# Kernel tuning notes

Measured on AMD Instinct MI355X. Metric: run time of the kernel, lower is better.

## Reference

```python
import jax, jax.numpy as jnp
import numpy as np

B, T, S, H = 4, 2048, 2048, 1024


def setup_inputs() -> dict:
    key = jax.random.key(0)
    k1, k2, k3, k4, k5, k6 = jax.random.split(key, 6)
    scale_w = 1.0 / np.sqrt(H)  # roughly nn.Linear init scale
    return {
        "tar": jax.random.normal(k1, (B, T, H), jnp.float32),
        "src": jax.random.normal(k2, (B, S, H), jnp.float32),
        "ori_src": jax.random.normal(k3, (B, S, H), jnp.float32),
        "Wq": jax.random.normal(k4, (H, H), jnp.float32) * scale_w,
        "Wk": jax.random.normal(k5, (H, H), jnp.float32) * scale_w,
        "Wv": jax.random.normal(k6, (H, H), jnp.float32) * scale_w,
    }


def reference(tar, src, ori_src, Wq, Wk, Wv):
    # nn.Linear(bias=False): y = x @ W.T
    q = src @ Wq.T        # (B, S, H)
    k = tar @ Wk.T        # (B, T, H)
    v = ori_src @ Wv.T    # (B, S, H)
    scaling = jnp.asarray(H ** 0.5, q.dtype)
    # scores[b,t,s] = q[b,s] . k[b,t] / sqrt(H); torch softmax was over dim=-2 (the S axis)
    scores = jnp.einsum('bsh,bth->bts', q, k) / scaling  # (B, T, S)
    attn = jax.nn.softmax(scores, axis=-1)               # softmax over src positions s
    context = jnp.einsum('bts,bsh->bth', attn, v)        # (B, T, H)
    return context, attn
```

## Files before the change

### kernel.cpp

```cpp
#include <hip/hip_runtime.h>

#define BB 4
#define TT 2048
#define SS 2048
#define HH 1024

typedef unsigned short u16;
typedef __attribute__((ext_vector_type(4))) unsigned short u16x4;
typedef __attribute__((ext_vector_type(8))) short bf16x8;
typedef __attribute__((ext_vector_type(4))) float f32x4;

__device__ __forceinline__ u16 f2bf(float f) {
    union { float f; unsigned u; } a; a.f = f;
    unsigned r = a.u + 0x7fffu + ((a.u >> 16) & 1u);
    return (u16)(r >> 16);
}

__device__ __forceinline__ void stage_bf16(const u16* gbase, int ld, int row0, int k0,
                                           u16* lds, int tid) {
#pragma unroll
    for (int c = 0; c < 2; ++c) {
        int g = c * 256 + tid;
        int row = g >> 2, col = g & 3;
        const u16* gp = gbase + (size_t)(row0 + row) * ld + k0 + col * 8;
        u16* lp = lds + (size_t)(c * 256 + (tid & ~63)) * 8;
        __builtin_amdgcn_global_load_lds((__attribute__((address_space(1))) const void*)gp,
                                         (__attribute__((address_space(3))) void*)lp,
                                         16, 0, 0);
    }
}

__device__ __forceinline__ void stage_f32(const float* gbase, int ld, int row0, int k0,
                                          u16* lds, int tid) {
#pragma unroll
    for (int c = 0; c < 4; ++c) {
        int f = c * 256 + tid;
        int row = f >> 3, c4 = f & 7;
        const float4 v = *(const float4*)(gbase + (size_t)(row0 + row) * ld + k0 + c4 * 4);
        u16x4 o;
        o.x = f2bf(v.x); o.y = f2bf(v.y); o.z = f2bf(v.z); o.w = f2bf(v.w);
        *(u16x4*)(lds + row * 32 + c4 * 4) = o;
    }
}

__device__ __forceinline__ void mfma_step(const u16* As, const u16* Bs,
                                          f32x4 acc[4][4], int tid) {
    int lane = tid & 63, quad = lane >> 4, l16 = lane & 15;
    int wm = (tid >> 6) & 1, wn = tid >> 7;
    const u16* Ab = As + (wm * 64 + l16) * 32 + quad * 8;
    const u16* Bb = Bs + (wn * 64 + l16) * 32 + quad * 8;
    bf16x8 af[4], bfr[4];
#pragma unroll
    for (int i = 0; i < 4; ++i) af[i] = *(const bf16x8*)(Ab + i * 512);
#pragma unroll
    for (int j = 0; j < 4; ++j) bfr[j] = *(const bf16x8*)(Bb + j * 512);
#pragma unroll
    for (int i = 0; i < 4; ++i)
#pragma unroll
        for (int j = 0; j < 4; ++j)
            acc[i][j] = __builtin_amdgcn_mfma_f32_16x16x32_bf16(af[i], bfr[j], acc[i][j], 0, 0, 0);
}

__device__ __forceinline__ void zero_acc(f32x4 acc[4][4]) {
#pragma unroll
    for (int i = 0; i < 4; ++i)
#pragma unroll
        for (int j = 0; j < 4; ++j)
            acc[i][j] = (f32x4){0.f, 0.f, 0.f, 0.f};
}

__global__ __launch_bounds__(256) void cvt_kernel(const float* __restrict__ in,
                                                  u16* __restrict__ out) {
    int i = (blockIdx.x * 256 + threadIdx.x) * 4;
    float4 v = *(const float4*)(in + i);
    u16x4 o;
    o.x = f2bf(v.x); o.y = f2bf(v.y); o.z = f2bf(v.z); o.w = f2bf(v.w);
    *(u16x4*)(out + i) = o;
}

template <int AF32>
__global__ __launch_bounds__(256) void proj_kernel(const float* __restrict__ F0,
                                                   const float* __restrict__ F1,
                                                   const float* __restrict__ F2,
                                                   const u16* __restrict__ A0,
                                                   const u16* __restrict__ A1,
                                                   const u16* __restrict__ A2,
                                                   const u16* __restrict__ W0,
                                                   const u16* __restrict__ W1,
                                                   const u16* __restrict__ W2,
                                                   u16* __restrict__ qb,
                                                   u16* __restrict__ kb,
                                                   u16* __restrict__ vT,
                                                   int zbase) {
    __shared__ u16 As[128 * 32];
    __shared__ u16 Bs[128 * 32];
    const int z = zbase + blockIdx.z;
    const float* AF = (z == 0) ? F0 : (z == 1) ? F1 : F2;
    const u16* AB = (z == 0) ? A0 : (z == 1) ? A1 : A2;
    const u16* W = (z == 0) ? W0 : (z == 1) ? W1 : W2;
    const int bm = blockIdx.y * 128, bn = blockIdx.x * 128;
    const int tid = threadIdx.x;

    f32x4 acc[4][4];
    zero_acc(acc);
    for (int k0 = 0; k0 < HH; k0 += 32) {
        if (AF32) stage_f32(AF, HH, bm, k0, As, tid);
        else      stage_bf16(AB, HH, bm, k0, As, tid);
        stage_bf16(W, HH, bn, k0, Bs, tid);
        __syncthreads();
        mfma_step(As, Bs, acc, tid);
        __syncthreads();
    }

    const int lane = tid & 63, quad = lane >> 4, l16 = lane & 15;
    const int wm = (tid >> 6) & 1, wn = tid >> 7;
    const int m0 = bm + wm * 64, n0 = bn + wn * 64;
    if (z < 2) {
        u16* C = (z == 0) ? qb : kb;
#pragma unroll
        for (int i = 0; i < 4; ++i)
#pragma unroll
            for (int j = 0; j < 4; ++j) {
                int m = m0 + i * 16 + quad * 4;
                int n = n0 + j * 16 + l16;
#pragma unroll
                for (int r = 0; r < 4; ++r)
                    C[(size_t)(m + r) * HH + n] = f2bf(acc[i][j][r]);
            }
    } else {
#pragma unroll
        for (int i = 0; i < 4; ++i)
#pragma unroll
            for (int j = 0; j < 4; ++j) {
                int m = m0 + i * 16 + quad * 4;
                int n = n0 + j * 16 + l16;
                u16x4 o;
                o.x = f2bf(acc[i][j][0]); o.y = f2bf(acc[i][j][1]);
                o.z = f2bf(acc[i][j][2]); o.w = f2bf(acc[i][j][3]);
                *(u16x4*)(vT + (size_t)n * (BB * SS) + m) = o;
            }
    }
}

__global__ __launch_bounds__(256) void scores_kernel(const u16* __restrict__ qb,
                                                     const u16* __restrict__ kb,
                                                     float* __restrict__ attn) {
    __shared__ u16 As[128 * 32];
    __shared__ u16 Bs[128 * 32];
    const int b = blockIdx.z;
    const u16* A = kb + (size_t)b * TT * HH;
    const u16* Bq = qb + (size_t)b * SS * HH;
    float* C = attn + (size_t)b * TT * SS;
    const int bm = blockIdx.y * 128, bn = blockIdx.x * 128;
    const int tid = threadIdx.x;

    f32x4 acc[4][4];
    zero_acc(acc);
    for (int k0 = 0; k0 < HH; k0 += 32) {
        stage_bf16(A, HH, bm, k0, As, tid);
        stage_bf16(Bq, HH, bn, k0, Bs, tid);
        __syncthreads();
        mfma_step(As, Bs, acc, tid);
        __syncthreads();
    }

    const int lane = tid & 63, quad = lane >> 4, l16 = lane & 15;
    const int wm = (tid >> 6) & 1, wn = tid >> 7;
    const int m0 = bm + wm * 64, n0 = bn + wn * 64;
#pragma unroll
    for (int i = 0; i < 4; ++i)
#pragma unroll
        for (int j = 0; j < 4; ++j) {
            int m = m0 + i * 16 + quad * 4;
            int n = n0 + j * 16 + l16;
#pragma unroll
            for (int r = 0; r < 4; ++r)
                C[(size_t)(m + r) * SS + n] = acc[i][j][r] * 0.03125f;
        }
}

__global__ __launch_bounds__(256) void softmax_kernel(float* __restrict__ attn,
                                                      u16* __restrict__ attn_bf) {
    const size_t row = blockIdx.x;
    float* p = attn + row * SS;
    const int tid = threadIdx.x;
    float4 a = *(float4*)(p + tid * 4);
    float4 b = *(float4*)(p + 1024 + tid * 4);

    float m = fmaxf(fmaxf(fmaxf(a.x, a.y), fmaxf(a.z, a.w)),
                    fmaxf(fmaxf(b.x, b.y), fmaxf(b.z, b.w)));
#pragma unroll
    for (int off = 32; off > 0; off >>= 1) m = fmaxf(m, __shfl_xor(m, off, 64));
    __shared__ float rmax[4], rsum[4];
    if ((tid & 63) == 0) rmax[tid >> 6] = m;
    __syncthreads();
    m = fmaxf(fmaxf(rmax[0], rmax[1]), fmaxf(rmax[2], rmax[3]));

    a.x = __expf(a.x - m); a.y = __expf(a.y - m);
    a.z = __expf(a.z - m); a.w = __expf(a.w - m);
    b.x = __expf(b.x - m); b.y = __expf(b.y - m);
    b.z = __expf(b.z - m); b.w = __expf(b.w - m);
    float s = a.x + a.y + a.z + a.w + b.x + b.y + b.z + b.w;
#pragma unroll
    for (int off = 32; off > 0; off >>= 1) s += __shfl_xor(s, off, 64);
    if ((tid & 63) == 0) rsum[tid >> 6] = s;
    __syncthreads();
    s = rsum[0] + rsum[1] + rsum[2] + rsum[3];
    float inv = 1.0f / s;

    a.x *= inv; a.y *= inv; a.z *= inv; a.w *= inv;
    b.x *= inv; b.y *= inv; b.z *= inv; b.w *= inv;
    *(float4*)(p + tid * 4) = a;
    *(float4*)(p + 1024 + tid * 4) = b;

    if (attn_bf) {
        u16* pb = attn_bf + row * SS;
        u16x4 oa, ob;
        oa.x = f2bf(a.x); oa.y = f2bf(a.y); oa.z = f2bf(a.z); oa.w = f2bf(a.w);
        ob.x = f2bf(b.x); ob.y = f2bf(b.y); ob.z = f2bf(b.z); ob.w = f2bf(b.w);
        *(u16x4*)(pb + tid * 4) = oa;
        *(u16x4*)(pb + 1024 + tid * 4) = ob;
    }
}

template <int AF32>
__global__ __launch_bounds__(256) void ctx_kernel(const float* __restrict__ attnF,
                                                  const u16* __restrict__ attnB,
                                                  const u16* __restrict__ vT,
                                                  float* __restrict__ out) {
    __shared__ u16 As[128 * 32];
    __shared__ u16 Bs[128 * 32];
    const int b = blockIdx.z;
    const float* AF = attnF + (size_t)b * TT * SS;
    const u16* AB = attnB + (size_t)b * TT * SS;
    const u16* Bv = vT + (size_t)b * SS;
    float* C = out + (size_t)b * TT * HH;
    const int bm = blockIdx.y * 128, bn = blockIdx.x * 128;
    const int tid = threadIdx.x;

    f32x4 acc[4][4];
    zero_acc(acc);
    for (int k0 = 0; k0 < SS; k0 += 32) {
        if (AF32) stage_f32(AF, SS, bm, k0, As, tid);
        else      stage_bf16(AB, SS, bm, k0, As, tid);
        stage_bf16(Bv, BB * SS, bn, k0, Bs, tid);
        __syncthreads();
        mfma_step(As, Bs, acc, tid);
        __syncthreads();
    }

    const int lane = tid & 63, quad = lane >> 4, l16 = lane & 15;
    const int wm = (tid >> 6) & 1, wn = tid >> 7;
    const int m0 = bm + wm * 64, n0 = bn + wn * 64;
#pragma unroll
    for (int i = 0; i < 4; ++i)
#pragma unroll
        for (int j = 0; j < 4; ++j) {
            int m = m0 + i * 16 + quad * 4;
            int n = n0 + j * 16 + l16;
#pragma unroll
            for (int r = 0; r < 4; ++r)
                C[(size_t)(m + r) * HH + n] = acc[i][j][r];
        }
}

extern "C" void kernel_launch(void* const* d_in, const int* in_sizes, int n_in,
                              void* d_out, int out_size, void* d_ws, size_t ws_size,
                              hipStream_t stream) {
    const float* tar = (const float*)d_in[0];
    const float* src = (const float*)d_in[1];
    const float* ori = (const float*)d_in[2];
    const float* Wq  = (const float*)d_in[3];
    const float* Wk  = (const float*)d_in[4];
    const float* Wv  = (const float*)d_in[5];

    float* ctx_out  = (float*)d_out;
    float* attn_out = ctx_out + (size_t)BB * TT * HH;

    const size_t M1 = 1024 * 1024;
    u16* ws  = (u16*)d_ws;
    u16* qb  = ws;
    u16* kb  = ws + 8 * M1;
    u16* vT  = ws + 16 * M1;
    u16* wqb = ws + 24 * M1;
    u16* wkb = ws + 25 * M1;
    u16* wvb = ws + 26 * M1;
    u16* inb = ws + 27 * M1;
    u16* attn_bf = qb;

    const size_t need_fused = (27 + 24) * M1 * 2;
    const size_t need_split = (27 + 8) * M1 * 2;
    const int mode = (ws_size >= need_fused) ? 0 : (ws_size >= need_split) ? 1 : 2;

    cvt_kernel<<<1024, 256, 0, stream>>>(Wq, wqb);
    cvt_kernel<<<1024, 256, 0, stream>>>(Wk, wkb);
    cvt_kernel<<<1024, 256, 0, stream>>>(Wv, wvb);

    if (mode == 0) {
        u16* srcb = inb;
        u16* tarb = inb + 8 * M1;
        u16* orib = inb + 16 * M1;
        cvt_kernel<<<8192, 256, 0, stream>>>(src, srcb);
        cvt_kernel<<<8192, 256, 0, stream>>>(tar, tarb);
        cvt_kernel<<<8192, 256, 0, stream>>>(ori, orib);
        proj_kernel<0><<<dim3(HH / 128, (BB * SS) / 128, 3), 256, 0, stream>>>(
            nullptr, nullptr, nullptr, srcb, tarb, orib, wqb, wkb, wvb, qb, kb, vT, 0);
    } else if (mode == 1) {
        const float* fin[3] = {src, tar, ori};
        for (int z = 0; z < 3; ++z) {
            cvt_kernel<<<8192, 256, 0, stream>>>(fin[z], inb);
            proj_kernel<0><<<dim3(HH / 128, (BB * SS) / 128, 1), 256, 0, stream>>>(
                nullptr, nullptr, nullptr, inb, inb, inb, wqb, wkb, wvb, qb, kb, vT, z);
        }
    } else {
        proj_kernel<1><<<dim3(HH / 128, (BB * SS) / 128, 3), 256, 0, stream>>>(
            src, tar, ori, nullptr, nullptr, nullptr, wqb, wkb, wvb, qb, kb, vT, 0);
    }

    scores_kernel<<<dim3(SS / 128, TT / 128, BB), 256, 0, stream>>>(qb, kb, attn_out);

    softmax_kernel<<<BB * TT, 256, 0, stream>>>(attn_out, (mode < 2) ? attn_bf : nullptr);

    if (mode < 2) {
        ctx_kernel<0><<<dim3(HH / 128, TT / 128, BB), 256, 0, stream>>>(
            nullptr, attn_bf, vT, ctx_out);
    } else {
        ctx_kernel<1><<<dim3(HH / 128, TT / 128, BB), 256, 0, stream>>>(
            attn_out, nullptr, vT, ctx_out);
    }
}
```

Baseline: 412.2 us.

## Double-buffer LDS tiles in GEMM loops and batch conversion launches

```diff
diff --git a/kernel.cpp b/kernel.cpp
--- a/kernel.cpp
+++ b/kernel.cpp
@@ -9,6 +9,8 @@
 typedef __attribute__((ext_vector_type(4))) unsigned short u16x4;
 typedef __attribute__((ext_vector_type(8))) short bf16x8;
 typedef __attribute__((ext_vector_type(4))) float f32x4;
+
+#define TILE_U16 (128 * 32)
 
 __device__ __forceinline__ u16 f2bf(float f) {
     union { float f; unsigned u; } a; a.f = f;
@@ -69,6 +71,58 @@
             acc[i][j] = (f32x4){0.f, 0.f, 0.f, 0.f};
 }
 
+__device__ __forceinline__ void gemm_loop_bf16(const u16* A, int lda, int bm,
+                                               const u16* B, int ldb, int bn,
+                                               int K, u16* As, u16* Bs,
+                                               f32x4 acc[4][4], int tid) {
+    stage_bf16(A, lda, bm, 0, As, tid);
+    stage_bf16(B, ldb, bn, 0, Bs, tid);
+    const int kiters = K / 32;
+    for (int kit = 0; kit < kiters; ++kit) {
+        const int cur = (kit & 1) * TILE_U16, nxt = TILE_U16 - cur;
+        __syncthreads();
+        if (kit + 1 < kiters) {
+            stage_bf16(A, lda, bm, (kit + 1) * 32, As + nxt, tid);
+            stage_bf16(B, ldb, bn, (kit + 1) * 32, Bs + nxt, tid);
+        }
+        mfma_step(As + cur, Bs + cur, acc, tid);
+    }
+}
+
+__device__ __forceinline__ void gemm_loop_f32a(const float* A, int lda, int bm,
+                                               const u16* B, int ldb, int bn,
+                                               int K, u16* As, u16* Bs,
+                                               f32x4 acc[4][4], int tid) {
+    stage_f32(A, lda, bm, 0, As, tid);
+    stage_bf16(B, ldb, bn, 0, Bs, tid);
+    const int kiters = K / 32;
+    for (int kit = 0; kit < kiters; ++kit) {
+        const int cur = (kit & 1) * TILE_U16, nxt = TILE_U16 - cur;
+        __syncthreads();
+        if (kit + 1 < kiters) {
+            stage_f32(A, lda, bm, (kit + 1) * 32, As + nxt, tid);
+            stage_bf16(B, ldb, bn, (kit + 1) * 32, Bs + nxt, tid);
+        }
+        mfma_step(As + cur, Bs + cur, acc, tid);
+    }
+}
+
+__global__ __launch_bounds__(256) void cvt3_kernel(const float* __restrict__ p0,
+                                                   const float* __restrict__ p1,
+                                                   const float* __restrict__ p2,
+                                                   u16* __restrict__ o0,
+                                                   u16* __restrict__ o1,
+                                                   u16* __restrict__ o2) {
+    const int z = blockIdx.y;
+    const float* in = (z == 0) ? p0 : (z == 1) ? p1 : p2;
+    u16* out = (z == 0) ? o0 : (z == 1) ? o1 : o2;
+    int i = (blockIdx.x * 256 + threadIdx.x) * 4;
+    float4 v = *(const float4*)(in + i);
+    u16x4 o;
+    o.x = f2bf(v.x); o.y = f2bf(v.y); o.z = f2bf(v.z); o.w = f2bf(v.w);
+    *(u16x4*)(out + i) = o;
+}
+
 __global__ __launch_bounds__(256) void cvt_kernel(const float* __restrict__ in,
                                                   u16* __restrict__ out) {
     int i = (blockIdx.x * 256 + threadIdx.x) * 4;
@@ -79,21 +133,21 @@
 }
 
 template <int AF32>
-__global__ __launch_bounds__(256) void proj_kernel(const float* __restrict__ F0,
-                                                   const float* __restrict__ F1,
-                                                   const float* __restrict__ F2,
-                                                   const u16* __restrict__ A0,
-                                                   const u16* __restrict__ A1,
-                                                   const u16* __restrict__ A2,
-                                                   const u16* __restrict__ W0,
-                                                   const u16* __restrict__ W1,
-                                                   const u16* __restrict__ W2,
-                                                   u16* __restrict__ qb,
-                                                   u16* __restrict__ kb,
-                                                   u16* __restrict__ vT,
-                                                   int zbase) {
-    __shared__ u16 As[128 * 32];
-    __shared__ u16 Bs[128 * 32];
+__global__ __launch_bounds__(256, 4) void proj_kernel(const float* __restrict__ F0,
+                                                      const float* __restrict__ F1,
+                                                      const float* __restrict__ F2,
+                                                      const u16* __restrict__ A0,
+                                                      const u16* __restrict__ A1,
+                                                      const u16* __restrict__ A2,
+                                                      const u16* __restrict__ W0,
+                                                      const u16* __restrict__ W1,
+                                                      const u16* __restrict__ W2,
+                                                      u16* __restrict__ qb,
+                                                      u16* __restrict__ kb,
+                                                      u16* __restrict__ vT,
+                                                      int zbase) {
+    __shared__ u16 As[2 * TILE_U16];
+    __shared__ u16 Bs[2 * TILE_U16];
     const int z = zbase + blockIdx.z;
     const float* AF = (z == 0) ? F0 : (z == 1) ? F1 : F2;
     const u16* AB = (z == 0) ? A0 : (z == 1) ? A1 : A2;
@@ -103,14 +157,8 @@
 
     f32x4 acc[4][4];
     zero_acc(acc);
-    for (int k0 = 0; k0 < HH; k0 += 32) {
-        if (AF32) stage_f32(AF, HH, bm, k0, As, tid);
-        else      stage_bf16(AB, HH, bm, k0, As, tid);
-        stage_bf16(W, HH, bn, k0, Bs, tid);
-        __syncthreads();
-        mfma_step(As, Bs, acc, tid);
-        __syncthreads();
-    }
+    if (AF32) gemm_loop_f32a(AF, HH, bm, W, HH, bn, HH, As, Bs, acc, tid);
+    else      gemm_loop_bf16(AB, HH, bm, W, HH, bn, HH, As, Bs, acc, tid);
 
     const int lane = tid & 63, quad = lane >> 4, l16 = lane & 15;
     const int wm = (tid >> 6) & 1, wn = tid >> 7;
@@ -142,11 +190,11 @@
     }
 }
 
-__global__ __launch_bounds__(256) void scores_kernel(const u16* __restrict__ qb,
-                                                     const u16* __restrict__ kb,
-                                                     float* __restrict__ attn) {
-    __shared__ u16 As[128 * 32];
-    __shared__ u16 Bs[128 * 32];
+__global__ __launch_bounds__(256, 4) void scores_kernel(const u16* __restrict__ qb,
+                                                        const u16* __restrict__ kb,
+                                                        float* __restrict__ attn) {
+    __shared__ u16 As[2 * TILE_U16];
+    __shared__ u16 Bs[2 * TILE_U16];
     const int b = blockIdx.z;
     const u16* A = kb + (size_t)b * TT * HH;
     const u16* Bq = qb + (size_t)b * SS * HH;
@@ -156,13 +204,7 @@
 
     f32x4 acc[4][4];
     zero_acc(acc);
-    for (int k0 = 0; k0 < HH; k0 += 32) {
-        stage_bf16(A, HH, bm, k0, As, tid);
-        stage_bf16(Bq, HH, bn, k0, Bs, tid);
-        __syncthreads();
-        mfma_step(As, Bs, acc, tid);
-        __syncthreads();
-    }
+    gemm_loop_bf16(A, HH, bm, Bq, HH, bn, HH, As, Bs, acc, tid);
 
     const int lane = tid & 63, quad = lane >> 4, l16 = lane & 15;
     const int wm = (tid >> 6) & 1, wn = tid >> 7;
@@ -224,12 +266,12 @@
 }
 
 template <int AF32>
-__global__ __launch_bounds__(256) void ctx_kernel(const float* __restrict__ attnF,
-                                                  const u16* __restrict__ attnB,
-                                                  const u16* __restrict__ vT,
-                                                  float* __restrict__ out) {
-    __shared__ u16 As[128 * 32];
-    __shared__ u16 Bs[128 * 32];
+__global__ __launch_bounds__(256, 4) void ctx_kernel(const float* __restrict__ attnF,
+                                                     const u16* __restrict__ attnB,
+                                                     const u16* __restrict__ vT,
+                                                     float* __restrict__ out) {
+    __shared__ u16 As[2 * TILE_U16];
+    __shared__ u16 Bs[2 * TILE_U16];
     const int b = blockIdx.z;
     const float* AF = attnF + (size_t)b * TT * SS;
     const u16* AB = attnB + (size_t)b * TT * SS;
@@ -240,14 +282,8 @@
 
     f32x4 acc[4][4];
     zero_acc(acc);
-    for (int k0 = 0; k0 < SS; k0 += 32) {
-        if (AF32) stage_f32(AF, SS, bm, k0, As, tid);
-        else      stage_bf16(AB, SS, bm, k0, As, tid);
-        stage_bf16(Bv, BB * SS, bn, k0, Bs, tid);
-        __syncthreads();
-        mfma_step(As, Bs, acc, tid);
-        __syncthreads();
-    }
+    if (AF32) gemm_loop_f32a(AF, SS, bm, Bv, BB * SS, bn, SS, As, Bs, acc, tid);
+    else      gemm_loop_bf16(AB, SS, bm, Bv, BB * SS, bn, SS, As, Bs, acc, tid);
 
     const int lane = tid & 63, quad = lane >> 4, l16 = lane & 15;
     const int wm = (tid >> 6) & 1, wn = tid >> 7;
@@ -292,17 +328,13 @@
     const size_t need_split = (27 + 8) * M1 * 2;
     const int mode = (ws_size >= need_fused) ? 0 : (ws_size >= need_split) ? 1 : 2;
 
-    cvt_kernel<<<1024, 256, 0, stream>>>(Wq, wqb);
-    cvt_kernel<<<1024, 256, 0, stream>>>(Wk, wkb);
-    cvt_kernel<<<1024, 256, 0, stream>>>(Wv, wvb);
+    cvt3_kernel<<<dim3(1024, 3), 256, 0, stream>>>(Wq, Wk, Wv, wqb, wkb, wvb);
 
     if (mode == 0) {
         u16* srcb = inb;
         u16* tarb = inb + 8 * M1;
         u16* orib = inb + 16 * M1;
-        cvt_kernel<<<8192, 256, 0, stream>>>(src, srcb);
-        cvt_kernel<<<8192, 256, 0, stream>>>(tar, tarb);
-        cvt_kernel<<<8192, 256, 0, stream>>>(ori, orib);
+        cvt3_kernel<<<dim3(8192, 3), 256, 0, stream>>>(src, tar, ori, srcb, tarb, orib);
         proj_kernel<0><<<dim3(HH / 128, (BB * SS) / 128, 3), 256, 0, stream>>>(
             nullptr, nullptr, nullptr, srcb, tarb, orib, wqb, wkb, wvb, qb, kb, vT, 0);
     } else if (mode == 1) {
```

Measured after the change: 383.1 us. -7.1%, faster.
